# Optimization experiments

Measured on AMD Instinct MI355X. Metric: run time of the kernel, lower is better.

## Reference

```python
import jax, jax.numpy as jnp
import numpy as np

T, B = 64, 32
V, E, H = 32000, 1024, 1024


def setup_inputs() -> dict:
    key = jax.random.key(0)
    ks = jax.random.split(key, 8)
    return {
        "target_tokens": jax.random.randint(ks[0], (T, B), 0, V),
        "ground_truth": jax.random.randint(ks[1], (T, B), 0, V),
        "embedding": jax.random.normal(ks[2], (V, E), jnp.float32) * 0.02,
        "W_ih": jax.random.normal(ks[3], (E, 4 * H), jnp.float32) / np.sqrt(E),
        "W_hh": jax.random.normal(ks[4], (H, 4 * H), jnp.float32) / np.sqrt(H),
        "b": jnp.zeros((4 * H,), jnp.float32),
        "W_out": jax.random.normal(ks[5], (H, V), jnp.float32) / np.sqrt(H),
        "b_out": jnp.zeros((V,), jnp.float32),
    }


def _lstm_logits(emb, W_ih, W_hh, b, W_out, b_out):
    # emb: [T, B, E] time-major; initial state (H_C=None) -> zeros
    Bsz = emb.shape[1]
    h0 = jnp.zeros((Bsz, W_hh.shape[0]), emb.dtype)
    c0 = jnp.zeros_like(h0)
    # precompute input projection for all timesteps in one GEMM
    x_proj = jnp.einsum('tbe,eg->tbg', emb, W_ih) + b  # [T, B, 4H]

    def step(carry, xg):
        h, c = carry
        gates = xg + h @ W_hh  # [B, 4H]
        i, f, g, o = jnp.split(gates, 4, axis=-1)
        c = jax.nn.sigmoid(f) * c + jax.nn.sigmoid(i) * jnp.tanh(g)
        h = jax.nn.sigmoid(o) * jnp.tanh(c)
        return (h, c), h

    (_, _), hs = jax.lax.scan(step, (h0, c0), x_proj)  # hs: [T, B, H]
    logits = jnp.einsum('tbh,hv->tbv', hs, W_out) + b_out  # [T, B, V]
    return logits


def reference(target_tokens, ground_truth, embedding, W_ih, W_hh, b, W_out, b_out):
    emb = embedding[target_tokens]  # [T, B, E]
    logits = _lstm_logits(emb, W_ih, W_hh, b, W_out, b_out)
    logits2d = logits.reshape(-1, logits.shape[-1])  # [T*B, V]
    gt = ground_truth.reshape(-1)  # [T*B]
    logp = jax.nn.log_softmax(logits2d, axis=-1)
    nll = -jnp.take_along_axis(logp, gt[:, None], axis=1)[:, 0]
    return jnp.mean(nll)
```

## Files before the change

kernel.cpp:

```cpp
#include <hip/hip_runtime.h>
#include <hip/hip_bf16.h>

typedef unsigned short u16;
typedef unsigned char u8;
typedef unsigned long long ull;
typedef __attribute__((ext_vector_type(8))) short bf16x8;
typedef __attribute__((ext_vector_type(4))) float f32x4;
typedef __attribute__((ext_vector_type(4))) int i32x4;
typedef __attribute__((ext_vector_type(8))) int i32x8;

#define NSLICE 500

__device__ __forceinline__ u16 f2bf(float x){
  unsigned b = __float_as_uint(x);
  return (u16)((b + 0x7FFFu + ((b>>16)&1u)) >> 16);
}
__device__ __forceinline__ float sigm(float x){ return 1.f/(1.f+__expf(-x)); }

__device__ __forceinline__ void gload_lds16(const void* g, void* l){
  __builtin_amdgcn_global_load_lds(
      (const __attribute__((address_space(1))) unsigned int*)g,
      (__attribute__((address_space(3))) unsigned int*)l, 16, 0, 0);
}
#define SWZ(row, kb) ((kb) ^ (((row)&7)<<4))

template<int OFF>
__device__ __forceinline__ i32x4 gload16_coh(const char* p){
  i32x4 d;
  asm volatile("global_load_dwordx4 %0, %1, off offset:%2 sc0 sc1"
               : "=v"(d) : "v"(p), "n"(OFF) : "memory");
  return d;
}

__device__ __forceinline__ f32x4 mfma_f8(i32x8 a, i32x8 b, f32x4 c){
  asm("v_mfma_f32_16x16x128_f8f6f4 %0, %1, %2, %0" : "+v"(c) : "v"(a), "v"(b));
  return c;
}

__device__ __forceinline__ void load_tile64(
    const float* __restrict__ in, int N, int nb, int kb, float (*tile)[65])
{
  const int t = threadIdx.x;
#pragma unroll
  for (int i=0;i<4;++i){
    int idx = i*256 + t;
    int k = idx>>4, n4 = idx&15;
    const float4 v = *(const float4*)&in[(size_t)(kb+k)*N + nb + n4*4];
    tile[k][n4*4+0]=v.x; tile[k][n4*4+1]=v.y; tile[k][n4*4+2]=v.z; tile[k][n4*4+3]=v.w;
  }
  __syncthreads();
}

__global__ __launch_bounds__(256) void prep_kernel(
    const float* __restrict__ Wout, const float* __restrict__ Wih,
    const float* __restrict__ Whh, const int* __restrict__ tok,
    const float* __restrict__ emb,
    u8* __restrict__ WoutT8, u16* __restrict__ WihT, u16* __restrict__ WhhT,
    u16* __restrict__ embg, float* __restrict__ zbuf, float* __restrict__ out0)
{
  __shared__ float tile[64][65];
  const int b = blockIdx.x;
  const int t = threadIdx.x;
  if (b < 8000){
    const int nb = (b%500)*64, kb = (b/500)*64;
    load_tile64(Wout, 32000, nb, kb, tile);
#pragma unroll
    for (int i=0;i<2;++i){
      int idx = i*256 + t;
      int n = idx>>3, k8 = idx&7;
      float v0=tile[k8*8+0][n], v1=tile[k8*8+1][n], v2=tile[k8*8+2][n], v3=tile[k8*8+3][n];
      float v4=tile[k8*8+4][n], v5=tile[k8*8+5][n], v6=tile[k8*8+6][n], v7=tile[k8*8+7][n];
      unsigned w0 = __builtin_amdgcn_cvt_pk_fp8_f32(v0, v1, 0, 0);
      w0 = __builtin_amdgcn_cvt_pk_fp8_f32(v2, v3, w0, 1);
      unsigned w1 = __builtin_amdgcn_cvt_pk_fp8_f32(v4, v5, 0, 0);
      w1 = __builtin_amdgcn_cvt_pk_fp8_f32(v6, v7, w1, 1);
      *(ull*)&WoutT8[(size_t)(nb+n)*1024 + kb + k8*8] = (ull)w0 | ((ull)w1<<32);
    }
  } else if (b < 10048){
    const int i = (b < 9024) ? b - 8000 : b - 9024;
    const float* in = (b < 9024) ? Wih : Whh;
    u16* out = (b < 9024) ? WihT : WhhT;
    const int nb = (i&63)*64, kb = (i>>6)*64;
    load_tile64(in, 4096, nb, kb, tile);
#pragma unroll
    for (int ii=0;ii<2;++ii){
      int idx = ii*256 + t;
      int n = idx>>3, k8 = idx&7;
      u16 tmp[8];
#pragma unroll
      for (int jj=0;jj<8;++jj) tmp[jj] = f2bf(tile[k8*8+jj][n]);
      *(ulonglong2*)&out[(size_t)(nb+n)*1024 + kb + k8*8] = *(ulonglong2*)tmp;
    }
  } else if (b < 12096){
    const int r = b - 10048;
    const int trow = tok[r];
    const float4 v = *(const float4*)(emb + (size_t)trow*1024 + t*4);
    ull o = (ull)f2bf(v.x) | ((ull)f2bf(v.y)<<16) | ((ull)f2bf(v.z)<<32) | ((ull)f2bf(v.w)<<48);
    *(ull*)(embg + (size_t)r*1024 + t*4) = o;
  } else {
    const int i = (b - 12096)*256 + t;
    if (i < 65792) zbuf[i] = 0.f;
    if (i == 0) out0[0] = 0.f;
  }
}

__device__ __forceinline__ void gemm_tile_128(
    const u16* __restrict__ A, const u16* __restrict__ BT,
    int rowbase, int colbase, u16* As, u16* Bs, f32x4 (&acc)[4][4])
{
  const int tid = threadIdx.x;
  const int lane = tid & 63;
  const int wm = (tid>>6)>>1, wn = (tid>>6)&1;
#pragma unroll
  for (int m=0;m<4;++m)
#pragma unroll
    for (int n=0;n<4;++n) acc[m][n] = (f32x4){0.f,0.f,0.f,0.f};

  for (int kb = 0; kb < 1024; kb += 64){
    __syncthreads();
#pragma unroll
    for (int i=0;i<4;++i){
      const int row = i*32 + (tid>>3);
      const int kf  = (tid&7)*16;
      gload_lds16((const char*)(A  + (size_t)(rowbase+row)*1024 + kb) + SWZ(row,kf),
                  (char*)As + (i*256+tid)*16);
      gload_lds16((const char*)(BT + (size_t)(colbase+row)*1024 + kb) + SWZ(row,kf),
                  (char*)Bs + (i*256+tid)*16);
    }
    __syncthreads();
#pragma unroll
    for (int ks=0;ks<2;++ks){
      bf16x8 af[4], bfr[4];
      const int kbyte = ks*64 + (lane>>4)*16;
#pragma unroll
      for (int m=0;m<4;++m){
        const int row = wm*64 + m*16 + (lane&15);
        af[m] = *(const bf16x8*)((const char*)As + row*128 + SWZ(row,kbyte));
      }
#pragma unroll
      for (int n=0;n<4;++n){
        const int col = wn*64 + n*16 + (lane&15);
        bfr[n] = *(const bf16x8*)((const char*)Bs + col*128 + SWZ(col,kbyte));
      }
#pragma unroll
      for (int m=0;m<4;++m)
#pragma unroll
        for (int n=0;n<4;++n)
          acc[m][n] = __builtin_amdgcn_mfma_f32_16x16x32_bf16(af[m], bfr[n], acc[m][n], 0,0,0);
    }
  }
}

__global__ __launch_bounds__(256,2) void xproj_gemm(
    const u16* __restrict__ Aemb, const u16* __restrict__ WihT,
    const float* __restrict__ bias, float* __restrict__ xgP)
{
  __shared__ u16 As[8192], Bs[8192];
  const int fb = blockIdx.x;
  const int g = (fb&7)*64 + (fb>>3);
  const int ct = g>>4, rt = g&15;
  const int rowbase = rt*128, colbase = ct*128;
  const int tid = threadIdx.x, lane = tid&63;
  const int wm = (tid>>6)>>1, wn = (tid>>6)&1;
  f32x4 acc[4][4];
  gemm_tile_128(Aemb, WihT, rowbase, colbase, As, Bs, acc);
  float bv[4];
#pragma unroll
  for (int n=0;n<4;++n) bv[n] = bias[colbase + wn*64 + n*16 + (lane&15)];
#pragma unroll
  for (int m=0;m<4;++m)
#pragma unroll
    for (int n=0;n<4;++n)
#pragma unroll
      for (int r=0;r<4;++r){
        const int row = rowbase + wm*64 + m*16 + (lane>>4)*4 + r;
        const int col = colbase + wn*64 + n*16 + (lane&15);
        const int tt = row>>5, b = row&31;
        const int q = col>>10, hcol = col&1023;
        xgP[(size_t)(((tt*256 + (hcol>>2))*32 + b)*16 + (hcol&3)*4 + q)] = acc[m][n][r] + bv[n];
      }
}

__global__ __launch_bounds__(256,1) void lstm_persistent(
    const u16* __restrict__ WhhT, const float* __restrict__ xgP,
    u16* __restrict__ hb0, u16* __restrict__ hb1, u8* __restrict__ hsf8,
    unsigned* __restrict__ bar)
{
  __shared__ float red[4*32*16];
  const int cb = blockIdx.x;
  const int tid = threadIdx.x, lane = tid&63, w = tid>>6;
  const int f = lane & 15;
  const int kfrag = (lane>>4)*8;
  const int gcol = cb*4 + (f&3) + 1024*(f>>2);
  const int bb = tid>>2, j = tid&3;
  const int w8 = w*8;

  bf16x8 wreg[8];
#pragma unroll
  for (int i=0;i<8;++i)
    wreg[i] = *(const bf16x8*)(WhhT + (size_t)gcol*1024 + (w8+i)*32 + kfrag);

  float creg = 0.f;
  float4 x4 = {0.f,0.f,0.f,0.f};
  if (tid < 128)
    x4 = *(const float4*)(xgP + ((size_t)0*256 + cb)*512 + bb*16 + j*4);

  for (int t=0; t<64; ++t){
    const u16* hin = (t&1) ? hb1 : hb0;
    u16*      hout = (t&1) ? hb0 : hb1;

    const char* p0 = (const char*)(hin + (size_t)f*1024 + w8*32 + kfrag);
    const char* p1 = p0 + 32768;
    i32x4 h0[8], h1[8];
    h0[0]=gload16_coh<  0>(p0); h0[1]=gload16_coh< 64>(p0);
    h0[2]=gload16_coh<128>(p0); h0[3]=gload16_coh<192>(p0);
    h0[4]=gload16_coh<256>(p0); h0[5]=gload16_coh<320>(p0);
    h0[6]=gload16_coh<384>(p0); h0[7]=gload16_coh<448>(p0);
    h1[0]=gload16_coh<  0>(p1); h1[1]=gload16_coh< 64>(p1);
    h1[2]=gload16_coh<128>(p1); h1[3]=gload16_coh<192>(p1);
    h1[4]=gload16_coh<256>(p1); h1[5]=gload16_coh<320>(p1);
    h1[6]=gload16_coh<384>(p1); h1[7]=gload16_coh<448>(p1);
    asm volatile("s_waitcnt vmcnt(0)" ::: "memory");
    __builtin_amdgcn_sched_barrier(0);

    f32x4 acc0 = (f32x4){0.f,0.f,0.f,0.f};
    f32x4 acc1 = (f32x4){0.f,0.f,0.f,0.f};
#pragma unroll
    for (int i=0;i<8;++i){
      acc0 = __builtin_amdgcn_mfma_f32_16x16x32_bf16(
                 __builtin_bit_cast(bf16x8, h0[i]), wreg[i], acc0, 0,0,0);
      acc1 = __builtin_amdgcn_mfma_f32_16x16x32_bf16(
                 __builtin_bit_cast(bf16x8, h1[i]), wreg[i], acc1, 0,0,0);
    }
#pragma unroll
    for (int r=0;r<4;++r){
      red[w*512 + ((lane>>4)*4 + r)*16 + f]      = acc0[r];
      red[w*512 + (16 + (lane>>4)*4 + r)*16 + f] = acc1[r];
    }
    __syncthreads();
    unsigned hu = 0, fb8 = 0;
    if (tid < 128){
      float g4[4];
#pragma unroll
      for (int q=0;q<4;++q){
        const int ff = j + 4*q;
        g4[q] = red[0*512 + bb*16 + ff] + red[1*512 + bb*16 + ff]
              + red[2*512 + bb*16 + ff] + red[3*512 + bb*16 + ff];
      }
      g4[0] += x4.x; g4[1] += x4.y; g4[2] += x4.z; g4[3] += x4.w;
      const float iv = sigm(g4[0]), fv = sigm(g4[1]);
      const float gv = tanhf(g4[2]), ov = sigm(g4[3]);
      const float cn = fv*creg + iv*gv;
      const float hv = ov*tanhf(cn);
      creg = cn;
      hu = (unsigned)f2bf(hv);
      fb8 = __builtin_amdgcn_cvt_pk_fp8_f32(hv, 0.f, 0, 0) & 0xffu;
    }
    const unsigned v1 = __shfl_down(hu, 1, 64);
    const unsigned v2 = __shfl_down(hu, 2, 64);
    const unsigned v3 = __shfl_down(hu, 3, 64);
    const ull p = (ull)hu | ((ull)v1<<16) | ((ull)v2<<32) | ((ull)v3<<48);
    const unsigned f1 = __shfl_down(fb8, 1, 64);
    const unsigned f2 = __shfl_down(fb8, 2, 64);
    const unsigned f3 = __shfl_down(fb8, 3, 64);
    const unsigned pf = fb8 | (f1<<8) | (f2<<16) | (f3<<24);
    if (tid < 128 && j == 0){
      __hip_atomic_store((ull*)&hout[bb*1024 + cb*4], p,
                         __ATOMIC_RELAXED, __HIP_MEMORY_SCOPE_AGENT);
    }
    if (t < 63){
      __syncthreads();
      if (tid == 0)
        __hip_atomic_fetch_add(&bar[(cb & 7)*32], 1u,
                               __ATOMIC_RELAXED, __HIP_MEMORY_SCOPE_AGENT);
      if (tid < 128 && j == 0)
        *(unsigned*)&hsf8[(size_t)t*32768 + bb*1024 + cb*4] = pf;
      if (tid < 128)
        x4 = *(const float4*)(xgP + ((size_t)(t+1)*256 + cb)*512 + bb*16 + j*4);
      if (tid == 0){
        const unsigned target = (unsigned)(t+1)*32u;
        for (;;){
          bool ok = true;
#pragma unroll
          for (int i=0;i<8;++i)
            ok &= (__hip_atomic_load(&bar[i*32], __ATOMIC_RELAXED,
                                     __HIP_MEMORY_SCOPE_AGENT) >= target);
          if (ok) break;
          __builtin_amdgcn_s_sleep(2);
        }
        asm volatile("" ::: "memory");
      }
      __syncthreads();
    } else {
      if (tid < 128 && j == 0)
        *(unsigned*)&hsf8[(size_t)63*32768 + bb*1024 + cb*4] = pf;
    }
  }
}

__global__ __launch_bounds__(256) void lstm_step_mfma(
    const u16* __restrict__ hin, const u16* __restrict__ WhhT,
    const float* __restrict__ xgPt, float* __restrict__ ccell,
    u16* __restrict__ hout, u8* __restrict__ hs8_t)
{
  __shared__ float red[4*32*16];
  const int cb = blockIdx.x;
  const int tid = threadIdx.x, lane = tid&63, w = tid>>6;
  const int f = lane & 15;
  const int gcol = cb*4 + (f&3) + 1024*(f>>2);
  const int kfrag = (lane>>4)*8;
  f32x4 acc0 = (f32x4){0.f,0.f,0.f,0.f};
  f32x4 acc1 = (f32x4){0.f,0.f,0.f,0.f};
  const int kb0 = w*256;
#pragma unroll
  for (int kk=0; kk<256; kk+=32){
    const int k = kb0 + kk + kfrag;
    const bf16x8 bfr = *(const bf16x8*)(WhhT + (size_t)gcol*1024 + k);
    const bf16x8 a0  = *(const bf16x8*)(hin + (size_t)f*1024 + k);
    const bf16x8 a1  = *(const bf16x8*)(hin + (size_t)(16+f)*1024 + k);
    acc0 = __builtin_amdgcn_mfma_f32_16x16x32_bf16(a0, bfr, acc0, 0,0,0);
    acc1 = __builtin_amdgcn_mfma_f32_16x16x32_bf16(a1, bfr, acc1, 0,0,0);
  }
#pragma unroll
  for (int r=0;r<4;++r){
    red[w*512 + ((lane>>4)*4 + r)*16 + f]      = acc0[r];
    red[w*512 + (16 + (lane>>4)*4 + r)*16 + f] = acc1[r];
  }
  __syncthreads();
  if (tid < 128){
    const int bb = tid >> 2, j = tid & 3;
    const int hcol = cb*4 + j;
    const float4 x4 = *(const float4*)(xgPt + (size_t)cb*512 + bb*16 + j*4);
    float g4[4];
#pragma unroll
    for (int q=0;q<4;++q){
      const int ff = j + 4*q;
      g4[q] = red[0*512 + bb*16 + ff] + red[1*512 + bb*16 + ff]
            + red[2*512 + bb*16 + ff] + red[3*512 + bb*16 + ff];
    }
    g4[0] += x4.x; g4[1] += x4.y; g4[2] += x4.z; g4[3] += x4.w;
    const float iv = sigm(g4[0]), fv = sigm(g4[1]);
    const float gv = tanhf(g4[2]), ov = sigm(g4[3]);
    const int hidx = bb*1024 + hcol;
    const float cn = fv*ccell[hidx] + iv*gv;
    const float hv = ov*tanhf(cn);
    ccell[hidx] = cn;
    hout[hidx] = f2bf(hv);
    hs8_t[hidx] = (u8)(__builtin_amdgcn_cvt_pk_fp8_f32(hv, 0.f, 0, 0) & 0xffu);
  }
}

__global__ __launch_bounds__(256,2) void logits_gemm_lse(
    const u8* __restrict__ hs8, const u8* __restrict__ WoutT8,
    const float* __restrict__ bout, const int* __restrict__ gt,
    float* __restrict__ partm, float* __restrict__ parts, float* __restrict__ gtl)
{
  __shared__ u8 As8[16384], Bs8[16384];
  __shared__ int gts[128];
  const int fb = blockIdx.x;
  const int g = (fb&7)*500 + (fb>>3);
  const int vt = g>>4, rt = g&15;
  const int rowbase = rt*128, colbase = vt*128;
  const int tid = threadIdx.x, lane = tid&63;
  const int wm = (tid>>6)>>1, wn = (tid>>6)&1;
  if (tid < 128) gts[tid] = gt[rowbase + tid];
  f32x4 acc[4][4];
#pragma unroll
  for (int m=0;m<4;++m)
#pragma unroll
    for (int n=0;n<4;++n) acc[m][n] = (f32x4){0.f,0.f,0.f,0.f};

  for (int kb = 0; kb < 8; ++kb){
    __syncthreads();
#pragma unroll
    for (int i=0;i<4;++i){
      const int row = i*32 + (tid>>3);
      const int kf  = (tid&7)*16;
      gload_lds16((const char*)(hs8    + (size_t)(rowbase+row)*1024 + kb*128) + SWZ(row,kf),
                  (char*)As8 + (i*256+tid)*16);
      gload_lds16((const char*)(WoutT8 + (size_t)(colbase+row)*1024 + kb*128) + SWZ(row,kf),
                  (char*)Bs8 + (i*256+tid)*16);
    }
    __syncthreads();
    const int kbyte = (lane>>4)*32;
    i32x8 af[4], bfr[4];
#pragma unroll
    for (int m=0;m<4;++m){
      const int row = wm*64 + m*16 + (lane&15);
      union { i32x8 v8; i32x4 v4[2]; } u;
      u.v4[0] = *(const i32x4*)(As8 + row*128 + SWZ(row, kbyte));
      u.v4[1] = *(const i32x4*)(As8 + row*128 + SWZ(row, kbyte+16));
      af[m] = u.v8;
    }
#pragma unroll
    for (int n=0;n<4;++n){
      const int col = wn*64 + n*16 + (lane&15);
      union { i32x8 v8; i32x4 v4[2]; } u;
      u.v4[0] = *(const i32x4*)(Bs8 + col*128 + SWZ(col, kbyte));
      u.v4[1] = *(const i32x4*)(Bs8 + col*128 + SWZ(col, kbyte+16));
      bfr[n] = u.v8;
    }
#pragma unroll
    for (int m=0;m<4;++m)
#pragma unroll
      for (int n=0;n<4;++n)
        acc[m][n] = mfma_f8(af[m], bfr[n], acc[m][n]);
  }

  float bv[4];
#pragma unroll
  for (int n=0;n<4;++n) bv[n] = bout[colbase + wn*64 + n*16 + (lane&15)];
#pragma unroll
  for (int m=0;m<4;++m)
#pragma unroll
    for (int n=0;n<4;++n)
#pragma unroll
      for (int r=0;r<4;++r) acc[m][n][r] += bv[n];
  float rm[4][4], rs[4][4];
#pragma unroll
  for (int m=0;m<4;++m)
#pragma unroll
    for (int r=0;r<4;++r){
      float mx = fmaxf(fmaxf(acc[m][0][r],acc[m][1][r]), fmaxf(acc[m][2][r],acc[m][3][r]));
      mx = fmaxf(mx, __shfl_xor(mx,1,16));
      mx = fmaxf(mx, __shfl_xor(mx,2,16));
      mx = fmaxf(mx, __shfl_xor(mx,4,16));
      mx = fmaxf(mx, __shfl_xor(mx,8,16));
      float sv = __expf(acc[m][0][r]-mx) + __expf(acc[m][1][r]-mx)
               + __expf(acc[m][2][r]-mx) + __expf(acc[m][3][r]-mx);
      sv += __shfl_xor(sv,1,16);
      sv += __shfl_xor(sv,2,16);
      sv += __shfl_xor(sv,4,16);
      sv += __shfl_xor(sv,8,16);
      rm[m][r]=mx; rs[m][r]=sv;
    }
  const int slice = vt*2 + wn;
  if ((lane&15)==0){
#pragma unroll
    for (int m=0;m<4;++m)
#pragma unroll
      for (int r=0;r<4;++r){
        const int rloc = wm*64 + m*16 + (lane>>4)*4 + r;
        partm[(size_t)slice*2048 + rowbase + rloc] = rm[m][r];
        parts[(size_t)slice*2048 + rowbase + rloc] = rs[m][r];
      }
  }
#pragma unroll
  for (int m=0;m<4;++m)
#pragma unroll
    for (int r=0;r<4;++r){
      const int rloc = wm*64 + m*16 + (lane>>4)*4 + r;
      const int gg = gts[rloc] - colbase - wn*64;
      if (gg >= 0 && gg < 64 && (gg&15)==(lane&15)){
        const int n = gg>>4;
        const float val = (n==0)?acc[m][0][r] : (n==1)?acc[m][1][r]
                        : (n==2)?acc[m][2][r] : acc[m][3][r];
        gtl[rowbase+rloc] = val;
      }
    }
}

__global__ __launch_bounds__(256) void lse_finalize2(
    const float* __restrict__ partm, const float* __restrict__ parts,
    const float* __restrict__ gtl, float* __restrict__ out)
{
  __shared__ float red[4];
  const int r = blockIdx.x*256 + threadIdx.x;
  float m = -1e30f;
  for (int i=0;i<NSLICE;++i) m = fmaxf(m, partm[(size_t)i*2048 + r]);
  float s = 0.f;
  for (int i=0;i<NSLICE;++i) s += parts[(size_t)i*2048 + r]*__expf(partm[(size_t)i*2048 + r]-m);
  float v = (m + logf(s) - gtl[r]) * (1.0f/2048.0f);
#pragma unroll
  for (int off=32;off>=1;off>>=1) v += __shfl_down(v, off, 64);
  if ((threadIdx.x&63)==0) red[threadIdx.x>>6]=v;
  __syncthreads();
  if (threadIdx.x==0) atomicAdd(out, red[0]+red[1]+red[2]+red[3]);
}

extern "C" void kernel_launch(void* const* d_in, const int* in_sizes, int n_in,
                              void* d_out, int out_size, void* d_ws, size_t ws_size,
                              hipStream_t stream)
{
  const int*   tok  = (const int*)d_in[0];
  const int*   gt   = (const int*)d_in[1];
  const float* emb  = (const float*)d_in[2];
  const float* Wih  = (const float*)d_in[3];
  const float* Whh  = (const float*)d_in[4];
  const float* bias = (const float*)d_in[5];
  const float* Wout = (const float*)d_in[6];
  const float* bout = (const float*)d_in[7];
  float* out = (float*)d_out;

  char* base = (char*)d_ws;
  u8*    WoutT8 = (u8*)base;            base += 32768000;
  u16*   WihT  = (u16*)base;            base += 8388608;
  u16*   WhhT  = (u16*)base;            base += 8388608;
  u16*   embg  = (u16*)base;            base += 4194304;
  float* xgP   = (float*)base;          base += 33554432;
  u8*    hsf8  = (u8*)base;             base += 2097152;
  float* cbuf  = (float*)base;          base += 131072;
  u16*   hb0   = (u16*)base;            base += 65536;
  u16*   hb1   = (u16*)base;            base += 65536;
  unsigned* bar = (unsigned*)base;      base += 1024;
  float* partm = (float*)base;          base += 4096000;
  float* parts = (float*)base;          base += 4096000;
  float* gtl   = (float*)base;          base += 8192;

  prep_kernel<<<12353, 256, 0, stream>>>(Wout, Wih, Whh, tok, emb,
                                         WoutT8, WihT, WhhT, embg, cbuf, out);

  xproj_gemm<<<512, 256, 0, stream>>>(embg, WihT, bias, xgP);

  int coop = 0;
  hipDeviceGetAttribute(&coop, hipDeviceAttributeCooperativeLaunch, 0);
  if (coop){
    void* args[] = {(void*)&WhhT, (void*)&xgP, (void*)&hb0, (void*)&hb1,
                    (void*)&hsf8, (void*)&bar};
    hipLaunchCooperativeKernel((const void*)lstm_persistent,
                               dim3(256), dim3(256), args, 0, stream);
  } else {
    for (int t = 0; t < 64; ++t){
      const u16* hin = (t & 1) ? hb1 : hb0;
      u16*      hout = (t & 1) ? hb0 : hb1;
      lstm_step_mfma<<<256, 256, 0, stream>>>(hin, WhhT,
          xgP + (size_t)t*131072, cbuf, hout, hsf8 + (size_t)t*32768);
    }
  }

  logits_gemm_lse<<<4000, 256, 0, stream>>>(hsf8, WoutT8, bout, gt, partm, parts, gtl);
  lse_finalize2<<<8, 256, 0, stream>>>(partm, parts, gtl, out);
}
```

Before: 570.4 us.

## Overlap Wout fp8 transpose with LSTM recurrence barrier waits

Moves the Wout fp32→fp8 transpose out of the prep kernel into the persistent LSTM kernel. Each block loads one 64x64 tile into LDS on even steps and converts/stores it on odd steps, using idle time around the inter-block barrier. This removes a large bandwidth-bound prep phase from the critical path. The per-step work and memory traffic of the latency-sensitive recurrence grow in exchange. The cooperative launch and per-step fallback path are also replaced by a plain launch, which relies on all 256 blocks being co-resident.

```diff
diff --git a/kernel.cpp b/kernel.cpp
--- a/kernel.cpp
+++ b/kernel.cpp
@@ -52,34 +52,18 @@
 }
 
 __global__ __launch_bounds__(256) void prep_kernel(
-    const float* __restrict__ Wout, const float* __restrict__ Wih,
-    const float* __restrict__ Whh, const int* __restrict__ tok,
-    const float* __restrict__ emb,
-    u8* __restrict__ WoutT8, u16* __restrict__ WihT, u16* __restrict__ WhhT,
+    const float* __restrict__ Wih, const float* __restrict__ Whh,
+    const int* __restrict__ tok, const float* __restrict__ emb,
+    u16* __restrict__ WihT, u16* __restrict__ WhhT,
     u16* __restrict__ embg, float* __restrict__ zbuf, float* __restrict__ out0)
 {
   __shared__ float tile[64][65];
   const int b = blockIdx.x;
   const int t = threadIdx.x;
-  if (b < 8000){
-    const int nb = (b%500)*64, kb = (b/500)*64;
-    load_tile64(Wout, 32000, nb, kb, tile);
-#pragma unroll
-    for (int i=0;i<2;++i){
-      int idx = i*256 + t;
-      int n = idx>>3, k8 = idx&7;
-      float v0=tile[k8*8+0][n], v1=tile[k8*8+1][n], v2=tile[k8*8+2][n], v3=tile[k8*8+3][n];
-      float v4=tile[k8*8+4][n], v5=tile[k8*8+5][n], v6=tile[k8*8+6][n], v7=tile[k8*8+7][n];
-      unsigned w0 = __builtin_amdgcn_cvt_pk_fp8_f32(v0, v1, 0, 0);
-      w0 = __builtin_amdgcn_cvt_pk_fp8_f32(v2, v3, w0, 1);
-      unsigned w1 = __builtin_amdgcn_cvt_pk_fp8_f32(v4, v5, 0, 0);
-      w1 = __builtin_amdgcn_cvt_pk_fp8_f32(v6, v7, w1, 1);
-      *(ull*)&WoutT8[(size_t)(nb+n)*1024 + kb + k8*8] = (ull)w0 | ((ull)w1<<32);
-    }
-  } else if (b < 10048){
-    const int i = (b < 9024) ? b - 8000 : b - 9024;
-    const float* in = (b < 9024) ? Wih : Whh;
-    u16* out = (b < 9024) ? WihT : WhhT;
+  if (b < 2048){
+    const int i = (b < 1024) ? b : b - 1024;
+    const float* in = (b < 1024) ? Wih : Whh;
+    u16* out = (b < 1024) ? WihT : WhhT;
     const int nb = (i&63)*64, kb = (i>>6)*64;
     load_tile64(in, 4096, nb, kb, tile);
 #pragma unroll
@@ -91,14 +75,14 @@
       for (int jj=0;jj<8;++jj) tmp[jj] = f2bf(tile[k8*8+jj][n]);
       *(ulonglong2*)&out[(size_t)(nb+n)*1024 + kb + k8*8] = *(ulonglong2*)tmp;
     }
-  } else if (b < 12096){
-    const int r = b - 10048;
+  } else if (b < 4096){
+    const int r = b - 2048;
     const int trow = tok[r];
     const float4 v = *(const float4*)(emb + (size_t)trow*1024 + t*4);
     ull o = (ull)f2bf(v.x) | ((ull)f2bf(v.y)<<16) | ((ull)f2bf(v.z)<<32) | ((ull)f2bf(v.w)<<48);
     *(ull*)(embg + (size_t)r*1024 + t*4) = o;
   } else {
-    const int i = (b - 12096)*256 + t;
+    const int i = (b - 4096)*256 + t;
     if (i < 65792) zbuf[i] = 0.f;
     if (i == 0) out0[0] = 0.f;
   }
@@ -184,9 +168,11 @@
 __global__ __launch_bounds__(256,1) void lstm_persistent(
     const u16* __restrict__ WhhT, const float* __restrict__ xgP,
     u16* __restrict__ hb0, u16* __restrict__ hb1, u8* __restrict__ hsf8,
-    unsigned* __restrict__ bar)
+    unsigned* __restrict__ bar,
+    const float* __restrict__ Wout, u8* __restrict__ WoutT8)
 {
   __shared__ float red[4*32*16];
+  __shared__ float tile[64][65];
   const int cb = blockIdx.x;
   const int tid = threadIdx.x, lane = tid&63, w = tid>>6;
   const int f = lane & 15;
@@ -268,6 +254,7 @@
       __hip_atomic_store((ull*)&hout[bb*1024 + cb*4], p,
                          __ATOMIC_RELAXED, __HIP_MEMORY_SCOPE_AGENT);
     }
+    const int tile_id = (t>>1)*256 + cb;
     if (t < 63){
       __syncthreads();
       if (tid == 0)
@@ -277,6 +264,32 @@
         *(unsigned*)&hsf8[(size_t)t*32768 + bb*1024 + cb*4] = pf;
       if (tid < 128)
         x4 = *(const float4*)(xgP + ((size_t)(t+1)*256 + cb)*512 + bb*16 + j*4);
+      if (tile_id < 8000){
+        const int nb = (tile_id % 500)*64, kb = (tile_id / 500)*64;
+        if ((t & 1) == 0){
+#pragma unroll
+          for (int i=0;i<4;++i){
+            int idx = i*256 + tid;
+            int k = idx>>4, n4 = idx&15;
+            const float4 v = *(const float4*)&Wout[(size_t)(kb+k)*32000 + nb + n4*4];
+            tile[k][n4*4+0]=v.x; tile[k][n4*4+1]=v.y;
+            tile[k][n4*4+2]=v.z; tile[k][n4*4+3]=v.w;
+          }
+        } else {
+#pragma unroll
+          for (int i=0;i<2;++i){
+            int idx = i*256 + tid;
+            int n = idx>>3, k8 = idx&7;
+            float v0=tile[k8*8+0][n], s1=tile[k8*8+1][n], s2=tile[k8*8+2][n], s3=tile[k8*8+3][n];
+            float v4=tile[k8*8+4][n], s5=tile[k8*8+5][n], s6=tile[k8*8+6][n], s7=tile[k8*8+7][n];
+            unsigned w0 = __builtin_amdgcn_cvt_pk_fp8_f32(v0, s1, 0, 0);
+            w0 = __builtin_amdgcn_cvt_pk_fp8_f32(s2, s3, w0, 1);
+            unsigned w1 = __builtin_amdgcn_cvt_pk_fp8_f32(v4, s5, 0, 0);
+            w1 = __builtin_amdgcn_cvt_pk_fp8_f32(s6, s7, w1, 1);
+            *(ull*)&WoutT8[(size_t)(nb+n)*1024 + kb + k8*8] = (ull)w0 | ((ull)w1<<32);
+          }
+        }
+      }
       if (tid == 0){
         const unsigned target = (unsigned)(t+1)*32u;
         for (;;){
@@ -294,59 +307,22 @@
     } else {
       if (tid < 128 && j == 0)
         *(unsigned*)&hsf8[(size_t)63*32768 + bb*1024 + cb*4] = pf;
-    }
-  }
-}
-
-__global__ __launch_bounds__(256) void lstm_step_mfma(
-    const u16* __restrict__ hin, const u16* __restrict__ WhhT,
-    const float* __restrict__ xgPt, float* __restrict__ ccell,
-    u16* __restrict__ hout, u8* __restrict__ hs8_t)
-{
-  __shared__ float red[4*32*16];
-  const int cb = blockIdx.x;
-  const int tid = threadIdx.x, lane = tid&63, w = tid>>6;
-  const int f = lane & 15;
-  const int gcol = cb*4 + (f&3) + 1024*(f>>2);
-  const int kfrag = (lane>>4)*8;
-  f32x4 acc0 = (f32x4){0.f,0.f,0.f,0.f};
-  f32x4 acc1 = (f32x4){0.f,0.f,0.f,0.f};
-  const int kb0 = w*256;
-#pragma unroll
-  for (int kk=0; kk<256; kk+=32){
-    const int k = kb0 + kk + kfrag;
-    const bf16x8 bfr = *(const bf16x8*)(WhhT + (size_t)gcol*1024 + k);
-    const bf16x8 a0  = *(const bf16x8*)(hin + (size_t)f*1024 + k);
-    const bf16x8 a1  = *(const bf16x8*)(hin + (size_t)(16+f)*1024 + k);
-    acc0 = __builtin_amdgcn_mfma_f32_16x16x32_bf16(a0, bfr, acc0, 0,0,0);
-    acc1 = __builtin_amdgcn_mfma_f32_16x16x32_bf16(a1, bfr, acc1, 0,0,0);
-  }
-#pragma unroll
-  for (int r=0;r<4;++r){
-    red[w*512 + ((lane>>4)*4 + r)*16 + f]      = acc0[r];
-    red[w*512 + (16 + (lane>>4)*4 + r)*16 + f] = acc1[r];
-  }
-  __syncthreads();
-  if (tid < 128){
-    const int bb = tid >> 2, j = tid & 3;
-    const int hcol = cb*4 + j;
-    const float4 x4 = *(const float4*)(xgPt + (size_t)cb*512 + bb*16 + j*4);
-    float g4[4];
-#pragma unroll
-    for (int q=0;q<4;++q){
-      const int ff = j + 4*q;
-      g4[q] = red[0*512 + bb*16 + ff] + red[1*512 + bb*16 + ff]
-            + red[2*512 + bb*16 + ff] + red[3*512 + bb*16 + ff];
-    }
-    g4[0] += x4.x; g4[1] += x4.y; g4[2] += x4.z; g4[3] += x4.w;
-    const float iv = sigm(g4[0]), fv = sigm(g4[1]);
-    const float gv = tanhf(g4[2]), ov = sigm(g4[3]);
-    const int hidx = bb*1024 + hcol;
-    const float cn = fv*ccell[hidx] + iv*gv;
-    const float hv = ov*tanhf(cn);
-    ccell[hidx] = cn;
-    hout[hidx] = f2bf(hv);
-    hs8_t[hidx] = (u8)(__builtin_amdgcn_cvt_pk_fp8_f32(hv, 0.f, 0, 0) & 0xffu);
+      if (tile_id < 8000){
+        const int nb = (tile_id % 500)*64, kb = (tile_id / 500)*64;
+#pragma unroll
+        for (int i=0;i<2;++i){
+          int idx = i*256 + tid;
+          int n = idx>>3, k8 = idx&7;
+          float v0=tile[k8*8+0][n], s1=tile[k8*8+1][n], s2=tile[k8*8+2][n], s3=tile[k8*8+3][n];
+          float v4=tile[k8*8+4][n], s5=tile[k8*8+5][n], s6=tile[k8*8+6][n], s7=tile[k8*8+7][n];
+          unsigned w0 = __builtin_amdgcn_cvt_pk_fp8_f32(v0, s1, 0, 0);
+          w0 = __builtin_amdgcn_cvt_pk_fp8_f32(s2, s3, w0, 1);
+          unsigned w1 = __builtin_amdgcn_cvt_pk_fp8_f32(v4, s5, 0, 0);
+          w1 = __builtin_amdgcn_cvt_pk_fp8_f32(s6, s7, w1, 1);
+          *(ull*)&WoutT8[(size_t)(nb+n)*1024 + kb + k8*8] = (ull)w0 | ((ull)w1<<32);
+        }
+      }
+    }
   }
 }
 
@@ -507,26 +483,13 @@
   float* parts = (float*)base;          base += 4096000;
   float* gtl   = (float*)base;          base += 8192;
 
-  prep_kernel<<<12353, 256, 0, stream>>>(Wout, Wih, Whh, tok, emb,
-                                         WoutT8, WihT, WhhT, embg, cbuf, out);
+  prep_kernel<<<4353, 256, 0, stream>>>(Wih, Whh, tok, emb,
+                                        WihT, WhhT, embg, cbuf, out);
 
   xproj_gemm<<<512, 256, 0, stream>>>(embg, WihT, bias, xgP);
 
-  int coop = 0;
-  hipDeviceGetAttribute(&coop, hipDeviceAttributeCooperativeLaunch, 0);
-  if (coop){
-    void* args[] = {(void*)&WhhT, (void*)&xgP, (void*)&hb0, (void*)&hb1,
-                    (void*)&hsf8, (void*)&bar};
-    hipLaunchCooperativeKernel((const void*)lstm_persistent,
-                               dim3(256), dim3(256), args, 0, stream);
-  } else {
-    for (int t = 0; t < 64; ++t){
-      const u16* hin = (t & 1) ? hb1 : hb0;
-      u16*      hout = (t & 1) ? hb0 : hb1;
-      lstm_step_mfma<<<256, 256, 0, stream>>>(hin, WhhT,
-          xgP + (size_t)t*131072, cbuf, hout, hsf8 + (size_t)t*32768);
-    }
-  }
+  lstm_persistent<<<256, 256, 0, stream>>>(WhhT, xgP, hb0, hb1, hsf8, bar,
+                                           Wout, WoutT8);
 
   logits_gemm_lse<<<4000, 256, 0, stream>>>(hsf8, WoutT8, bout, gt, partm, parts, gtl);
   lse_finalize2<<<8, 256, 0, stream>>>(partm, parts, gtl, out);
```

Result: faster. 529.1 us (-7.2%).
